# Optimization experiments

Hardware: AMD Instinct MI355X
Metric: run time of the kernel (lower is better)

## Reference

```python
import jax, jax.numpy as jnp
import numpy as np

# dims: recurrence runs over axis 0 (B steps), cell batch is T (faithful to the
# original code, which unpacks `length, batch_size, _ = input.size()` on a
# batch-first tensor).
B, T, D = 32, 2048, 256
H = 512 // 2          # per-direction hidden (hidden_dim // 2)
CS = 32               # chunk_size
N = H // CS           # n_chunk = 8
G = 4 * H + 2 * N     # gate width = 1040


def setup_inputs() -> dict:
    key = jax.random.key(0)
    ks = jax.random.split(key, 5)
    x = jax.random.normal(ks[0], (B, T, D), jnp.float32)
    # seq_lens: sorted int lengths in [1, T] (concrete numpy -> static gather)
    sl = np.sort(np.random.default_rng(0).integers(1, T + 1, size=B)).astype(np.int64)
    s_in = 1.0 / np.sqrt(D)
    s_h = 1.0 / np.sqrt(H)
    W_ih = jax.random.uniform(ks[1], (G, D), jnp.float32, -s_in, s_in)
    b_ih = jax.random.uniform(ks[2], (G,), jnp.float32, -s_in, s_in)
    W_hh = jax.random.uniform(ks[3], (G, H), jnp.float32, -s_h, s_h)
    b_hh = jax.random.uniform(ks[4], (G,), jnp.float32, -s_h, s_h)
    return {"embedded_text": x, "seq_lens": sl,
            "W_ih": W_ih, "b_ih": b_ih, "W_hh": W_hh, "b_hh": b_hh}


def _cumsoftmax(x):
    return jnp.cumsum(jax.nn.softmax(x, axis=-1), axis=-1)


def _run_onlstm(x, W_ih, b_ih, W_hh, b_hh):
    """x: (B, T, D) -> hidden states (B, T, H); scan over axis 0."""
    t_in = jnp.einsum('btd,gd->btg', x, W_ih) + b_ih  # precomputed ih, (B,T,G)
    h0 = jnp.zeros((T, H), x.dtype)
    c0 = jnp.zeros((T, N, CS), x.dtype)

    def step(carry, ti):
        hx, cx = carry
        gates = ti + hx @ W_hh.T + b_hh                 # (T, G)
        cin = 1.0 - _cumsoftmax(gates[:, :N])           # (T, N)
        cfg = _cumsoftmax(gates[:, N:2 * N])            # (T, N)
        rest = gates[:, 2 * N:].reshape(-1, 4 * N, CS)
        og, cg, ig, fg = jnp.split(rest, 4, axis=1)     # each (T, N, CS)
        ig = jax.nn.sigmoid(ig)
        fg = jax.nn.sigmoid(fg)
        cg = jnp.tanh(cg)
        og = jax.nn.sigmoid(og)
        cin3 = cin[:, :, None]
        cfg3 = cfg[:, :, None]
        ov = cfg3 * cin3
        fg = fg * ov + (cfg3 - ov)
        ig = ig * ov + (cin3 - ov)
        cy = fg * cx + ig * cg
        hy = (og * jnp.tanh(cy)).reshape(-1, H)
        return (hy, cy), hy

    _, hs = jax.lax.scan(step, (h0, c0), t_in)          # (B, T, H)
    return hs


def reference(embedded_text, seq_lens, W_ih, b_ih, W_hh, b_hh):
    # eval mode: nn.Dropout / LockedDropout are identity; dropconnect=0 -> plain weight
    out_f = _run_onlstm(embedded_text, W_ih, b_ih, W_hh, b_hh)
    # faithful quirk: 'bidirectional' pass flips the FEATURE dim, same weights
    out_b = _run_onlstm(embedded_text[..., ::-1], W_ih, b_ih, W_hh, b_hh)
    out = jnp.concatenate([out_f, out_b], axis=-1)      # (B, T, 2H)
    sl = np.asarray(seq_lens)
    rows = np.repeat(np.arange(sl.shape[0]), sl)
    cols = np.concatenate([np.arange(int(l)) for l in sl])
    return out[rows, cols]                              # (sum(seq_lens), 2H)
```

## Files before the change

kernel.cpp:

```cpp
#include <hip/hip_runtime.h>
#include <hip/hip_bf16.h>

#define B_  32
#define T_  2048
#define D_  256
#define H_  256
#define G_  1040

#define NSL 8
#define NRB 16
#define NMB 4
#define NKB 32
#define NF  5
#define CTRSTRIDE 64

#define NBXT  512
#define NBWSW 640
#define XLP   264

using bf16   = __hip_bfloat16;
using short8 = __attribute__((ext_vector_type(8))) short;
using f32x16 = __attribute__((ext_vector_type(16))) float;
using ull    = unsigned long long;

__device__ inline float sigmoidf_(float v) {
  return __fdividef(1.f, 1.f + __expf(-v));
}
__device__ inline float tanh_(float v) {
  v = fminf(fmaxf(v, -15.f), 15.f);
  float e = __expf(2.f * v);
  return __fdividef(e - 1.f, e + 1.f);
}
__device__ inline float bf2f(unsigned short u) {
  union { unsigned int i; float f; } c; c.i = ((unsigned int)u) << 16; return c.f;
}
__device__ inline float ldF(const void* p, size_t i, int isf) {
  return isf ? ((const float*)p)[i] : bf2f(((const unsigned short*)p)[i]);
}
__device__ inline short f2bs(float v) {
  bf16 h = __float2bfloat16(v);
  return *(short*)&h;
}

__global__ __launch_bounds__(256) void prep_all(
    const void* __restrict__ x, const int* __restrict__ sli,
    const void* __restrict__ W_ih, const void* __restrict__ b_ih,
    const void* __restrict__ W_hh, const void* __restrict__ b_hh,
    int* __restrict__ meta, float* __restrict__ bsum,
    bf16* __restrict__ xs, bf16* __restrict__ Wsw)
{
  __shared__ __align__(16) short xt[128 * XLP];
  const int tid = threadIdx.x;

  __shared__ int s_bad;
  if (tid == 0) s_bad = 0;
  __syncthreads();
  {
    const unsigned short* xh = (const unsigned short*)x;
    int bad = 0;
    #pragma unroll
    for (int j = 0; j < 4; ++j) {
      float f = bf2f(xh[tid * 4 + j]);
      if (!(fabsf(f) < 100.f)) bad = 1;
    }
    if (bad) atomicOr(&s_bad, 1);
  }
  __syncthreads();
  const int isf = s_bad;

  const int blk = blockIdx.x;

  if (blk == 0) {
    if (tid == 0) {
      meta[0] = isf;
      bool is64 = true;
      for (int i = 1; i < 32; i += 2) if (sli[i] != 0) is64 = false;
      int base = 0;
      for (int b = 0; b < B_; ++b) {
        int v = is64 ? sli[2 * b] : sli[b];
        meta[8 + b]  = v;
        meta[40 + b] = base;
        base += v;
      }
    }
    for (int i = tid; i < G_; i += 256)
      bsum[i] = ldF(b_ih, i, isf) + ldF(b_hh, i, isf);
    return;
  }

  if (blk < 1 + NBXT) {
    const int bi = blk - 1;
    const int b  = bi >> 4;
    const int rb = bi & 15;
    const unsigned short* xh = (const unsigned short*)x;
    const float* xf = (const float*)x;

    #pragma unroll
    for (int i = 0; i < 16; ++i) {
      const int li  = i * 256 + tid;
      const int tr  = li >> 5;
      const int col = (li & 31) * 8;
      const size_t src = ((size_t)b * T_ + rb * 128 + tr) * D_ + col;
      short8 v;
      if (!isf) {
        v = *(const short8*)(xh + src);
      } else {
        #pragma unroll
        for (int j = 0; j < 8; ++j) v[j] = f2bs(xf[src + j]);
      }
      *(short8*)&xt[tr * XLP + col] = v;
    }
    __syncthreads();

    bf16* xsBase = xs + ((size_t)b * 16 + rb) * (16 * 4 * 64 * 8);
    #pragma unroll
    for (int i = 0; i < 16; ++i) {
      const int oc     = i * 256 + tid;
      const int lane_o = oc & 63;
      const int mb     = (oc >> 6) & 3;
      const int kbx    = oc >> 8;
      const int tr  = mb * 32 + (lane_o & 31);
      const int col = kbx * 16 + (lane_o >> 5) * 8;
      short8 v = *(const short8*)&xt[tr * XLP + col];
      *(short8*)(xsBase + (size_t)oc * 8) = v;
    }
    return;
  }

  {
    const int idx = (blk - 1 - NBXT) * 256 + tid;
    const int lane = idx & 63;
    const int f    = (idx >> 6) % NF;
    const int kb   = (idx / (64 * NF)) % NKB;
    const int sl   = (idx / (64 * NF * NKB)) % NSL;
    const int d    = idx / (64 * NF * NKB * NSL);
    const int n    = lane & 31;
    const int k0   = kb * 16 + (lane >> 5) * 8;
    const int g = (f < 4) ? (16 + f * H_ + sl * 32 + n) : ((n < 16) ? n : -1);
    short8 v;
    #pragma unroll
    for (int j = 0; j < 8; ++j) {
      float val = 0.f;
      const int k = k0 + j;
      if (g >= 0)
        val = (k < D_) ? ldF(W_ih, (size_t)g * D_ + (d ? (D_ - 1 - k) : k), isf)
                       : ldF(W_hh, (size_t)g * H_ + (k - D_), isf);
      v[j] = f2bs(val);
    }
    *(short8*)(Wsw + (size_t)idx * 8) = v;
  }
}

__global__ __launch_bounds__(256, 1) void onlstm_persist(
    const short* __restrict__ xs, const short* __restrict__ Wsw,
    short* __restrict__ hs, float* __restrict__ cs,
    const float* __restrict__ bsum, void* __restrict__ out,
    const int* __restrict__ meta, int* __restrict__ ctr,
    int b_lo, int b_hi)
{
  __shared__ short Wl[NKB * 4 * 512];
  __shared__ __align__(16) short Ht[NMB][32][40];

  const int tid  = threadIdx.x;
  const int lane = tid & 63;
  const int w    = tid >> 6;

  const int lin = blockIdx.x;
  const int rb  = (lin & 7) + 8 * ((lin >> 3) >> 4);
  const int p   = (lin >> 3) & 15;
  const int d   = p >> 3;
  const int s   = p & 7;

  const int col   = lane & 31;
  const int khalf = lane >> 5;
  const int isf   = meta[0];

  const short* wsrc = Wsw + ((size_t)(d * NSL + s) * NKB) * (NF * 512);

  for (int i = tid; i < NKB * 4 * 64; i += 256) {
    const int kb = i >> 8, rem = i & 255, f = rem >> 6, l = rem & 63;
    *(short8*)&Wl[((kb * 4 + f) << 9) + (l << 3)] =
        *(const short8*)(wsrc + ((kb * 5 + f) << 9) + (l << 3));
  }
  __syncthreads();

  float bg[4];
  #pragma unroll
  for (int f = 0; f < 4; ++f) bg[f] = bsum[16 + f * H_ + s * 32 + col];
  const float c0b = (col < 16) ? bsum[col] : 0.f;

  const int e = s * 32 + col;

  int* gctr = ctr + (size_t)(d * NRB + rb) * CTRSTRIDE;
  const short* w4p = wsrc + 4 * 512 + lane * 8;

  float* csP = cs + (((size_t)(d * NSL + s) * NRB + rb) * NMB + w) * 1024 + lane;

  f32x16 creg;
  if (b_lo > 0) {
    #pragma unroll
    for (int r = 0; r < 16; ++r) creg[r] = csP[r * 64];
  } else {
    #pragma unroll
    for (int r = 0; r < 16; ++r) creg[r] = 0.f;
  }

  short8 xn[16];
  {
    const short* aPtr = xs + (((size_t)b_lo * NRB + rb) * 16 * NMB + w) * 512 + lane * 8;
    #pragma unroll
    for (int kb = 0; kb < 16; ++kb)
      xn[kb] = *(const short8*)(aPtr + (size_t)kb * 2048);
  }

  for (int b = b_lo; b < b_hi; ++b) {
    const int len_s  = meta[8 + b];
    const int base_s = meta[40 + b];
    const bool lastb = (b + 1 >= B_);

    f32x16 acc[NF];
    #pragma unroll
    for (int f = 0; f < NF; ++f)
      #pragma unroll
      for (int r = 0; r < 16; ++r) acc[f][r] = 0.f;

    {
      const short* aNext = xs + (((size_t)(b + 1) * NRB + rb) * 16 * NMB + w) * 512 + lane * 8;
      const bool pf = (b + 1 < b_hi);
      const short* w4q = w4p;
      short8 q0 = *(const short8*)(w4q);
      short8 q1 = *(const short8*)(w4q + 2560);
      short8 q2 = *(const short8*)(w4q + 5120);
      short8 wf[2][4];
      #pragma unroll
      for (int f = 0; f < 4; ++f)
        wf[0][f] = *(const short8*)&Wl[((0 * 4 + f) << 9) + (lane << 3)];
      #pragma unroll
      for (int kb = 0; kb < 16; ++kb) {
        const int cur = kb & 1;
        if (kb + 1 < 16) {
          #pragma unroll
          for (int f = 0; f < 4; ++f)
            wf[cur ^ 1][f] = *(const short8*)&Wl[(((kb + 1) * 4 + f) << 9) + (lane << 3)];
        }
        const short8 af = xn[kb];
        if (pf) xn[kb] = *(const short8*)(aNext + (size_t)kb * 2048);
        const short8 b4 = q0;
        q0 = q1; q1 = q2;
        if (kb < 13) q2 = *(const short8*)(w4q + (kb + 3) * 2560);
        #pragma unroll
        for (int f = 0; f < 4; ++f)
          acc[f] = __builtin_amdgcn_mfma_f32_32x32x16_bf16(af, wf[cur][f], acc[f], 0, 0, 0);
        acc[4] = __builtin_amdgcn_mfma_f32_32x32x16_bf16(af, b4, acc[4], 0, 0, 0);
      }
    }

    if (b) {
      if (tid == 0) {
        ull t0 = __builtin_amdgcn_s_memrealtime();
        while (__hip_atomic_load(gctr, __ATOMIC_RELAXED,
                                 __HIP_MEMORY_SCOPE_AGENT) < 8 * b) {
          __builtin_amdgcn_s_sleep(1);
          if (__builtin_amdgcn_s_memrealtime() - t0 > 40000000ull) break;
        }
      }
      __syncthreads();

      ull hfA[16], hfB[16];
      {
        const short* hbase = hs + (((size_t)(((b & 1) ^ 1) * 2 + d) * NRB + rb) * 16 * NMB + w) * 512;
        #pragma unroll
        for (int kb = 0; kb < 16; ++kb) {
          const ull* hp = (const ull*)(hbase + (size_t)kb * NMB * 512) + lane * 2;
          hfA[kb] = __hip_atomic_load(hp,     __ATOMIC_RELAXED, __HIP_MEMORY_SCOPE_AGENT);
          hfB[kb] = __hip_atomic_load(hp + 1, __ATOMIC_RELAXED, __HIP_MEMORY_SCOPE_AGENT);
        }
      }

      const short* w4q = w4p + 16 * 2560;
      short8 q0 = *(const short8*)(w4q);
      short8 q1 = *(const short8*)(w4q + 2560);
      short8 q2 = *(const short8*)(w4q + 5120);
      short8 wf[2][4];
      #pragma unroll
      for (int f = 0; f < 4; ++f)
        wf[0][f] = *(const short8*)&Wl[(((16 * 4) + f) << 9) + (lane << 3)];
      #pragma unroll
      for (int kb = 0; kb < 16; ++kb) {
        const int cur = kb & 1;
        if (kb + 1 < 16) {
          #pragma unroll
          for (int f = 0; f < 4; ++f)
            wf[cur ^ 1][f] = *(const short8*)&Wl[(((16 + kb + 1) * 4 + f) << 9) + (lane << 3)];
        }
        union { ull u[2]; short8 v; } af;
        af.u[0] = hfA[kb]; af.u[1] = hfB[kb];
        const short8 b4 = q0;
        q0 = q1; q1 = q2;
        if (kb < 13) q2 = *(const short8*)(w4q + (kb + 3) * 2560);
        #pragma unroll
        for (int f = 0; f < 4; ++f)
          acc[f] = __builtin_amdgcn_mfma_f32_32x32x16_bf16(af.v, wf[cur][f], acc[f], 0, 0, 0);
        acc[4] = __builtin_amdgcn_mfma_f32_32x32x16_bf16(af.v, b4, acc[4], 0, 0, 0);
      }
    }

    f32x16 gv, mx, Sv, Pv;
    #pragma unroll
    for (int r = 0; r < 16; ++r) gv[r] = acc[4][r] + c0b;
    #pragma unroll
    for (int r = 0; r < 16; ++r) mx[r] = gv[r];
    #pragma unroll
    for (int r = 0; r < 16; ++r) { float t = __shfl_xor(mx[r], 1); mx[r] = fmaxf(mx[r], t); }
    #pragma unroll
    for (int r = 0; r < 16; ++r) { float t = __shfl_xor(mx[r], 2); mx[r] = fmaxf(mx[r], t); }
    #pragma unroll
    for (int r = 0; r < 16; ++r) { float t = __shfl_xor(mx[r], 4); mx[r] = fmaxf(mx[r], t); }
    #pragma unroll
    for (int r = 0; r < 16; ++r) gv[r] = __expf(gv[r] - mx[r]);
    const bool pin = (lane & 7) <= s;
    #pragma unroll
    for (int r = 0; r < 16; ++r) { Sv[r] = gv[r]; Pv[r] = pin ? gv[r] : 0.f; }
    #pragma unroll
    for (int r = 0; r < 16; ++r) { Sv[r] += __shfl_xor(Sv[r], 1); Pv[r] += __shfl_xor(Pv[r], 1); }
    #pragma unroll
    for (int r = 0; r < 16; ++r) { Sv[r] += __shfl_xor(Sv[r], 2); Pv[r] += __shfl_xor(Pv[r], 2); }
    #pragma unroll
    for (int r = 0; r < 16; ++r) { Sv[r] += __shfl_xor(Sv[r], 4); Pv[r] += __shfl_xor(Pv[r], 4); }
    #pragma unroll
    for (int r = 0; r < 16; ++r) Pv[r] = __fdividef(Pv[r], Sv[r]);
    f32x16 cinv, cfgv;
    #pragma unroll
    for (int r = 0; r < 16; ++r) cinv[r] = 1.f - __shfl(Pv[r], khalf * 32);
    #pragma unroll
    for (int r = 0; r < 16; ++r) cfgv[r] = __shfl(Pv[r], khalf * 32 + 8);

    #pragma unroll
    for (int r = 0; r < 16; ++r) {
      const int row = (r & 3) + 8 * (r >> 2) + 4 * khalf;
      const float cin = cinv[r];
      const float cfg = cfgv[r];
      const float og = sigmoidf_(acc[0][r] + bg[0]);
      const float cg = tanh_   (acc[1][r] + bg[1]);
      const float ig = sigmoidf_(acc[2][r] + bg[2]);
      const float fg = sigmoidf_(acc[3][r] + bg[3]);
      const float ov = cfg * cin;
      const float f2 = fg * ov + (cfg - ov);
      const float i2 = ig * ov + (cin - ov);
      const float cy = f2 * creg[r] + i2 * cg;
      creg[r] = cy;
      const float hy = og * tanh_(cy);
      if (!lastb) Ht[w][row][col] = f2bs(hy);
      const int t = rb * 128 + w * 32 + row;
      if (t < len_s) {
        const size_t o = (size_t)(base_s + t) * (2 * H_) + (size_t)d * H_ + e;
        if (isf) ((float*)out)[o] = hy;
        else     ((bf16*)out)[o]  = __float2bfloat16(hy);
      }
    }

    if (!lastb) {
      const int m  = lane & 31;
      const int k8 = lane >> 5;
      short* hbase = hs + (((size_t)((b & 1) * 2 + d) * NRB + rb) * 16 * NMB + w) * 512;
      #pragma unroll
      for (int c = 0; c < 2; ++c) {
        ull lo = *(const ull*)&Ht[w][m][c * 16 + k8 * 8];
        ull hi = *(const ull*)&Ht[w][m][c * 16 + k8 * 8 + 4];
        ull* q = (ull*)(hbase + (size_t)(2 * s + c) * NMB * 512) + lane * 2;
        __hip_atomic_store(q,     lo, __ATOMIC_RELAXED, __HIP_MEMORY_SCOPE_AGENT);
        __hip_atomic_store(q + 1, hi, __ATOMIC_RELAXED, __HIP_MEMORY_SCOPE_AGENT);
      }
    }

    __syncthreads();
    if (tid == 0)
      __hip_atomic_fetch_add(gctr, 1, __ATOMIC_RELAXED, __HIP_MEMORY_SCOPE_AGENT);
  }

  if (b_hi < B_) {
    #pragma unroll
    for (int r = 0; r < 16; ++r) csP[r * 64] = creg[r];
  }
}

extern "C" void kernel_launch(void* const* d_in, const int* in_sizes, int n_in,
                              void* d_out, int out_size, void* d_ws, size_t ws_size,
                              hipStream_t stream)
{
  const void* x    = d_in[0];
  const int*  sl   = (const int*)d_in[1];
  const void* W_ih = d_in[2];
  const void* b_ih = d_in[3];
  const void* W_hh = d_in[4];
  const void* b_hh = d_in[5];

  char* ws = (char*)d_ws;
  size_t off = 0;
  auto alloc = [&](size_t bytes) {
    void* p = ws + off;
    off = (off + bytes + 255) & ~(size_t)255;
    return p;
  };
  int*   meta = (int*)  alloc(128 * sizeof(int));
  short* xs   = (short*)alloc((size_t)B_ * T_ * D_ * sizeof(short));
  short* Wsw  = (short*)alloc((size_t)2 * NSL * NKB * NF * 512 * sizeof(short));
  short* hs   = (short*)alloc((size_t)2 * 2 * T_ * H_ * sizeof(short));
  float* bsum = (float*)alloc((size_t)G_ * sizeof(float));
  int*   ctr  = (int*)  alloc((size_t)32 * CTRSTRIDE * sizeof(int));
  float* cs   = (float*)alloc((size_t)2 * NSL * NRB * NMB * 1024 * sizeof(float));
  const bool have_cs = (off <= ws_size);

  hipMemsetAsync(ctr, 0, (size_t)32 * CTRSTRIDE * sizeof(int), stream);

  prep_all<<<1 + NBXT + NBWSW, 256, 0, stream>>>(
      x, sl, W_ih, b_ih, W_hh, b_hh, meta, bsum, (bf16*)xs, (bf16*)Wsw);

  int b_lo = 0, b_hi = B_;
  void* args[] = {(void*)&xs, (void*)&Wsw, (void*)&hs, (void*)&cs, (void*)&bsum,
                  (void*)&d_out, (void*)&meta, (void*)&ctr, (void*)&b_lo, (void*)&b_hi};
  hipError_t ce = hipLaunchCooperativeKernel((const void*)onlstm_persist,
                                             dim3(256), dim3(256), args, 0, stream);
  if (ce != hipSuccess) {
    (void)hipGetLastError();
    if (have_cs) {
      for (int b = 0; b < B_; ++b)
        onlstm_persist<<<dim3(256), dim3(256), 0, stream>>>(
            xs, Wsw, hs, cs, bsum, d_out, meta, ctr, b, b + 1);
    } else {
      onlstm_persist<<<dim3(256), dim3(256), 0, stream>>>(
          xs, Wsw, hs, cs, bsum, d_out, meta, ctr, 0, B_);
    }
  }
}
```

Measured before the change: 611.6 us.

## Merge two row-blocks per workgroup with 512 threads sharing LDS weights

Each workgroup now has 8 waves covering two row-blocks (rb and rb+8) that share one LDS copy of the weight slice, so the grid shrinks from 256 to 128 blocks. Sync counters are re-indexed per (direction, row-block pair), and all per-wave offsets use the wave's position within its half. This halves the global weight-loading traffic and the number of blocks taking part in each step's synchronisation. In exchange, half of the CUs are left idle, per-CU compute doubles, and the 512-thread launch bound limits per-wave registers, which risks spills given the large accumulator and prefetch arrays.

```diff
diff --git a/kernel.cpp b/kernel.cpp
--- a/kernel.cpp
+++ b/kernel.cpp
@@ -151,7 +151,7 @@
   }
 }
 
-__global__ __launch_bounds__(256, 1) void onlstm_persist(
+__global__ __launch_bounds__(512, 1) void onlstm_persist(
     const short* __restrict__ xs, const short* __restrict__ Wsw,
     short* __restrict__ hs, float* __restrict__ cs,
     const float* __restrict__ bsum, void* __restrict__ out,
@@ -159,17 +159,20 @@
     int b_lo, int b_hi)
 {
   __shared__ short Wl[NKB * 4 * 512];
-  __shared__ __align__(16) short Ht[NMB][32][40];
+  __shared__ __align__(16) short Ht[8][32][40];
 
   const int tid  = threadIdx.x;
   const int lane = tid & 63;
   const int w    = tid >> 6;
+  const int mb   = w & 3;
+  const int half = w >> 2;
 
   const int lin = blockIdx.x;
-  const int rb  = (lin & 7) + 8 * ((lin >> 3) >> 4);
-  const int p   = (lin >> 3) & 15;
-  const int d   = p >> 3;
-  const int s   = p & 7;
+  const int rbp = lin & 7;
+  const int q   = lin >> 3;
+  const int s   = q & 7;
+  const int d   = q >> 3;
+  const int rb  = rbp + half * 8;
 
   const int col   = lane & 31;
   const int khalf = lane >> 5;
@@ -177,7 +180,7 @@
 
   const short* wsrc = Wsw + ((size_t)(d * NSL + s) * NKB) * (NF * 512);
 
-  for (int i = tid; i < NKB * 4 * 64; i += 256) {
+  for (int i = tid; i < NKB * 4 * 64; i += 512) {
     const int kb = i >> 8, rem = i & 255, f = rem >> 6, l = rem & 63;
     *(short8*)&Wl[((kb * 4 + f) << 9) + (l << 3)] =
         *(const short8*)(wsrc + ((kb * 5 + f) << 9) + (l << 3));
@@ -191,10 +194,10 @@
 
   const int e = s * 32 + col;
 
-  int* gctr = ctr + (size_t)(d * NRB + rb) * CTRSTRIDE;
+  int* gctr = ctr + (size_t)(d * 8 + rbp) * CTRSTRIDE;
   const short* w4p = wsrc + 4 * 512 + lane * 8;
 
-  float* csP = cs + (((size_t)(d * NSL + s) * NRB + rb) * NMB + w) * 1024 + lane;
+  float* csP = cs + (((size_t)(d * NSL + s) * NRB + rb) * NMB + mb) * 1024 + lane;
 
   f32x16 creg;
   if (b_lo > 0) {
@@ -207,7 +210,7 @@
 
   short8 xn[16];
   {
-    const short* aPtr = xs + (((size_t)b_lo * NRB + rb) * 16 * NMB + w) * 512 + lane * 8;
+    const short* aPtr = xs + (((size_t)b_lo * NRB + rb) * 16 * NMB + mb) * 512 + lane * 8;
     #pragma unroll
     for (int kb = 0; kb < 16; ++kb)
       xn[kb] = *(const short8*)(aPtr + (size_t)kb * 2048);
@@ -225,7 +228,7 @@
       for (int r = 0; r < 16; ++r) acc[f][r] = 0.f;
 
     {
-      const short* aNext = xs + (((size_t)(b + 1) * NRB + rb) * 16 * NMB + w) * 512 + lane * 8;
+      const short* aNext = xs + (((size_t)(b + 1) * NRB + rb) * 16 * NMB + mb) * 512 + lane * 8;
       const bool pf = (b + 1 < b_hi);
       const short* w4q = w4p;
       short8 q0 = *(const short8*)(w4q);
@@ -268,7 +271,7 @@
 
       ull hfA[16], hfB[16];
       {
-        const short* hbase = hs + (((size_t)(((b & 1) ^ 1) * 2 + d) * NRB + rb) * 16 * NMB + w) * 512;
+        const short* hbase = hs + (((size_t)(((b & 1) ^ 1) * 2 + d) * NRB + rb) * 16 * NMB + mb) * 512;
         #pragma unroll
         for (int kb = 0; kb < 16; ++kb) {
           const ull* hp = (const ull*)(hbase + (size_t)kb * NMB * 512) + lane * 2;
@@ -351,7 +354,7 @@
       creg[r] = cy;
       const float hy = og * tanh_(cy);
       if (!lastb) Ht[w][row][col] = f2bs(hy);
-      const int t = rb * 128 + w * 32 + row;
+      const int t = rb * 128 + mb * 32 + row;
       if (t < len_s) {
         const size_t o = (size_t)(base_s + t) * (2 * H_) + (size_t)d * H_ + e;
         if (isf) ((float*)out)[o] = hy;
@@ -362,14 +365,14 @@
     if (!lastb) {
       const int m  = lane & 31;
       const int k8 = lane >> 5;
-      short* hbase = hs + (((size_t)((b & 1) * 2 + d) * NRB + rb) * 16 * NMB + w) * 512;
+      short* hbase = hs + (((size_t)((b & 1) * 2 + d) * NRB + rb) * 16 * NMB + mb) * 512;
       #pragma unroll
       for (int c = 0; c < 2; ++c) {
         ull lo = *(const ull*)&Ht[w][m][c * 16 + k8 * 8];
         ull hi = *(const ull*)&Ht[w][m][c * 16 + k8 * 8 + 4];
-        ull* q = (ull*)(hbase + (size_t)(2 * s + c) * NMB * 512) + lane * 2;
-        __hip_atomic_store(q,     lo, __ATOMIC_RELAXED, __HIP_MEMORY_SCOPE_AGENT);
-        __hip_atomic_store(q + 1, hi, __ATOMIC_RELAXED, __HIP_MEMORY_SCOPE_AGENT);
+        ull* q2 = (ull*)(hbase + (size_t)(2 * s + c) * NMB * 512) + lane * 2;
+        __hip_atomic_store(q2,     lo, __ATOMIC_RELAXED, __HIP_MEMORY_SCOPE_AGENT);
+        __hip_atomic_store(q2 + 1, hi, __ATOMIC_RELAXED, __HIP_MEMORY_SCOPE_AGENT);
       }
     }
 
@@ -420,15 +423,15 @@
   void* args[] = {(void*)&xs, (void*)&Wsw, (void*)&hs, (void*)&cs, (void*)&bsum,
                   (void*)&d_out, (void*)&meta, (void*)&ctr, (void*)&b_lo, (void*)&b_hi};
   hipError_t ce = hipLaunchCooperativeKernel((const void*)onlstm_persist,
-                                             dim3(256), dim3(256), args, 0, stream);
+                                             dim3(128), dim3(512), args, 0, stream);
   if (ce != hipSuccess) {
     (void)hipGetLastError();
     if (have_cs) {
       for (int b = 0; b < B_; ++b)
-        onlstm_persist<<<dim3(256), dim3(256), 0, stream>>>(
+        onlstm_persist<<<dim3(128), dim3(512), 0, stream>>>(
             xs, Wsw, hs, cs, bsum, d_out, meta, ctr, b, b + 1);
     } else {
-      onlstm_persist<<<dim3(256), dim3(256), 0, stream>>>(
+      onlstm_persist<<<dim3(128), dim3(512), 0, stream>>>(
           xs, Wsw, hs, cs, bsum, d_out, meta, ctr, 0, B_);
     }
   }
```

Result: slower. 1.075 ms (+75.7%).
